# Performance work log

Hardware: AMD Instinct MI355X
Metric: run time of the kernel (lower is better)

Reference implementation:

```python
import jax, jax.numpy as jnp
import numpy as np

N, D, IN_DIM, H, L = 20000, 32, 3, 64, 3


def _lstm_agg(h_nodes, nbr_sorted, W_ih, W_hh, b_ih, b_hh):
    """Batched LSTM over each node's (sorted) neighbor sequence; returns final hidden state h_T."""
    n = h_nodes.shape[0]
    hidden = W_hh.shape[1]

    def step(carry, idx):
        h, c = carry
        x = h_nodes[idx]                                     # [N, in_d] irregular gather
        gates = x @ W_ih.T + h @ W_hh.T + b_ih + b_hh        # [N, 4H], torch gate order i,f,g,o
        i_g, f_g, g_g, o_g = jnp.split(gates, 4, axis=-1)
        c = jax.nn.sigmoid(f_g) * c + jax.nn.sigmoid(i_g) * jnp.tanh(g_g)
        h = jax.nn.sigmoid(o_g) * jnp.tanh(c)
        return (h, c), None

    init = (jnp.zeros((n, hidden), h_nodes.dtype), jnp.zeros((n, hidden), h_nodes.dtype))
    (h_T, _), _ = jax.lax.scan(step, init, nbr_sorted.T)      # scan over D neighbor slots
    return h_T


def _layer(h, nbr_sorted, W_ih, W_hh, b_ih, b_hh, Wl, bl):
    agg = _lstm_agg(h, nbr_sorted, W_ih, W_hh, b_ih, b_hh)    # [N, H]
    comb = jnp.concatenate([h, agg], axis=-1)                 # [N, in_d + H]
    return jax.nn.relu(comb @ Wl.T + bl)


def _forward(node_features, nbr, params, W_out, b_out):
    nbr_sorted = jnp.sort(nbr, axis=1)   # permutation-invariant ordering (Eq. 9)
    h = node_features
    for p in params:
        h = _layer(h, nbr_sorted, *p)
    return (h @ W_out.T + b_out).squeeze(-1)   # [N] per-node log-likelihood scores


def setup_inputs():
    key = jax.random.key(0)
    ks = jax.random.split(key, 40)
    inp = {}
    inp["node_features"] = jax.random.normal(ks[0], (N, IN_DIM), jnp.float32)
    inp["nbr"] = jax.random.randint(ks[1], (N, D), 0, N, jnp.int32)
    k = 2
    s = 1.0 / np.sqrt(H)
    for l in range(L):
        in_d = IN_DIM if l == 0 else H
        inp[f"W_ih{l}"] = (jax.random.normal(ks[k], (4 * H, in_d)) * (1.0 / np.sqrt(in_d))).astype(jnp.float32); k += 1
        inp[f"W_hh{l}"] = (jax.random.normal(ks[k], (4 * H, H)) * s).astype(jnp.float32); k += 1
        inp[f"b_ih{l}"] = (jax.random.normal(ks[k], (4 * H,)) * s).astype(jnp.float32); k += 1
        inp[f"b_hh{l}"] = (jax.random.normal(ks[k], (4 * H,)) * s).astype(jnp.float32); k += 1
        inp[f"Wl{l}"] = (jax.random.normal(ks[k], (H, in_d + H)) * (1.0 / np.sqrt(in_d + H))).astype(jnp.float32); k += 1
        inp[f"bl{l}"] = (jax.random.normal(ks[k], (H,)) * s).astype(jnp.float32); k += 1
    inp["W_out"] = (jax.random.normal(ks[k], (1, H)) * s).astype(jnp.float32); k += 1
    inp["b_out"] = jnp.zeros((1,), jnp.float32)
    return inp


def reference(node_features, nbr, W_ih0, W_hh0, b_ih0, b_hh0, Wl0, bl0, W_ih1, W_hh1, b_ih1, b_hh1, Wl1, bl1, W_ih2, W_hh2, b_ih2, b_hh2, Wl2, bl2, W_out, b_out):
    params = [
        (W_ih0, W_hh0, b_ih0, b_hh0, Wl0, bl0),
        (W_ih1, W_hh1, b_ih1, b_hh1, Wl1, bl1),
        (W_ih2, W_hh2, b_ih2, b_hh2, Wl2, bl2),
    ]
    return _forward(node_features, nbr, params, W_out, b_out)
```

## Files before the change

kernel.cpp:

```cpp
#include <hip/hip_runtime.h>
#include <hip/hip_bf16.h>

#define NN 20000
#define NG 1250
#define LOG2E 1.44269504088896f
#define TWOLOG2E 2.88539008177793f

typedef __attribute__((ext_vector_type(8))) short short8;
typedef __attribute__((ext_vector_type(4))) float floatx4;

__device__ __forceinline__ floatx4 MF(short8 a, short8 b, floatx4 c) {
    return __builtin_amdgcn_mfma_f32_16x16x32_bf16(a, b, c, 0, 0, 0);
}
__device__ __forceinline__ float ex2(float x) { return __builtin_amdgcn_exp2f(x); }
__device__ __forceinline__ float rcp(float x) { return __builtin_amdgcn_rcpf(x); }
__device__ __forceinline__ float clamp30(float x) {
    return __builtin_fminf(__builtin_fmaxf(x, -30.f), 30.f);
}
__device__ __forceinline__ unsigned short bf16r(float x) {
    return __builtin_bit_cast(unsigned short, __float2bfloat16(x));
}
__device__ __forceinline__ void lds_barrier() {
    asm volatile("s_waitcnt lgkmcnt(0)\n\ts_barrier" ::: "memory");
}
__device__ __forceinline__ int rowswz(int L) {
    return L ^ (((L >> 4) & 1) << 1) ^ ((L >> 3) & 1);
}

__device__ __forceinline__ void lstm_cell4(const floatx4* acc, float* cst,
                                           unsigned short* buf, int q, int u) {
    #pragma unroll
    for (int r = 0; r < 4; r++) {
        float gi = clamp30(acc[0][r]);
        float gf = clamp30(acc[1][r]);
        float gg = clamp30(acc[2][r]);
        float go = clamp30(acc[3][r]);
        float ei = ex2(-gi), ef = ex2(-gf), eg = ex2(-gg), eo = ex2(-go);
        float pf = 1.f + ef;
        float p  = (1.f + ei) * (1.f + eg);
        float num = fmaf(cst[r], p, (1.f - eg) * pf);
        float cm  = num * rcp(p * pf);
        cst[r] = cm;
        float ec = ex2(-clamp30(TWOLOG2E * cm));
        float h  = (1.f - ec) * rcp((1.f + eo) * (1.f + ec));
        int row = 4*q + r + 16*(u >> 3);
        buf[rowswz(row)*8 + (u & 7)] = bf16r(h);
    }
}

#define PREP_TOT (49152 + 49152 + 12288 + 12288 + 768 + 640000)
__global__ void prep_kernel(const float* __restrict__ x, const int* __restrict__ nbr,
    const float* __restrict__ Wih0, const float* __restrict__ Whh0,
    const float* __restrict__ bih0, const float* __restrict__ bhh0, const float* __restrict__ Wl0,
    const float* __restrict__ Wih1, const float* __restrict__ Whh1,
    const float* __restrict__ bih1, const float* __restrict__ bhh1, const float* __restrict__ Wl1,
    const float* __restrict__ Wih2, const float* __restrict__ Whh2,
    const float* __restrict__ bih2, const float* __restrict__ bhh2, const float* __restrict__ Wl2,
    unsigned short* __restrict__ Wih_p, unsigned short* __restrict__ Whh_p,
    unsigned short* __restrict__ Wlx_p, unsigned short* __restrict__ Wlh_p,
    float* __restrict__ bsum, unsigned short* __restrict__ x32, int* __restrict__ nbrT)
{
    int tid = blockIdx.x * 256 + threadIdx.x;
    if (tid < NN) {
        int v[32];
        const int4* src = (const int4*)(nbr + tid * 32);
        #pragma unroll
        for (int i = 0; i < 8; i++) {
            int4 t = src[i];
            v[4*i] = t.x; v[4*i+1] = t.y; v[4*i+2] = t.z; v[4*i+3] = t.w;
        }
        #pragma unroll
        for (int k = 2; k <= 32; k <<= 1)
            #pragma unroll
            for (int j = k >> 1; j > 0; j >>= 1)
                #pragma unroll
                for (int i = 0; i < 32; i++) {
                    int ixj = i ^ j;
                    if (ixj > i) {
                        bool up = (i & k) == 0;
                        int a = v[i], b = v[ixj];
                        bool sw = up ? (a > b) : (a < b);
                        if (sw) { v[i] = b; v[ixj] = a; }
                    }
                }
        int g = tid >> 4, m = tid & 15;
        int base = g * 512 + m;
        #pragma unroll
        for (int t = 0; t < 32; t++) nbrT[base + t * 16] = v[t];
    }
    for (int i = blockIdx.x * 256 + threadIdx.x; i < PREP_TOT; i += gridDim.x * 256) {
        int j = i;
        if (j < 49152) {
            int l = j >> 14, e = j & 16383;
            if (l == 0) {
                if (e < 8192) {
                    int col = e >> 5, k = e & 31;
                    float sc = (col >= 128 && col < 192) ? TWOLOG2E : LOG2E;
                    float v = (k < 3) ? Wih0[col*3 + k] * sc : 0.f;
                    Wih_p[e] = bf16r(v);
                }
            } else {
                int col = e >> 6, k = e & 63;
                const float* W = (l == 1) ? Wih1 : Wih2;
                float sc = (col >= 128 && col < 192) ? TWOLOG2E : LOG2E;
                Wih_p[l*16384 + e] = bf16r(W[col*64 + k] * sc);
            }
            continue;
        }
        j -= 49152;
        if (j < 49152) {
            int l = j >> 14, e = j & 16383;
            int col = e >> 6, k = e & 63;
            const float* W = (l == 0) ? Whh0 : ((l == 1) ? Whh1 : Whh2);
            float sc = (col >= 128 && col < 192) ? TWOLOG2E : LOG2E;
            Whh_p[l*16384 + e] = bf16r(W[col*64 + k] * sc);
            continue;
        }
        j -= 49152;
        if (j < 12288) {
            int l = j >> 12, e = j & 4095;
            if (l == 0) {
                if (e < 2048) {
                    int col = e >> 5, k = e & 31;
                    float v = (k < 3) ? Wl0[col*67 + k] : 0.f;
                    Wlx_p[e] = bf16r(v);
                }
            } else {
                int col = e >> 6, k = e & 63;
                const float* W = (l == 1) ? Wl1 : Wl2;
                Wlx_p[l*4096 + e] = bf16r(W[col*128 + k]);
            }
            continue;
        }
        j -= 12288;
        if (j < 12288) {
            int l = j >> 12, e = j & 4095;
            int col = e >> 6, k = e & 63;
            float v = (l == 0) ? Wl0[col*67 + 3 + k]
                               : ((l == 1) ? Wl1 : Wl2)[col*128 + 64 + k];
            Wlh_p[l*4096 + e] = bf16r(v);
            continue;
        }
        j -= 12288;
        if (j < 768) {
            int l = j >> 8, col = j & 255;
            const float* bi = (l == 0) ? bih0 : ((l == 1) ? bih1 : bih2);
            const float* bh = (l == 0) ? bhh0 : ((l == 1) ? bhh1 : bhh2);
            float sc = (col >= 128 && col < 192) ? TWOLOG2E : LOG2E;
            bsum[l*256 + col] = (bi[col] + bh[col]) * sc;
            continue;
        }
        j -= 768;
        {
            int n = j >> 5, k = j & 31;
            x32[j] = bf16r((k < 3) ? x[n*3 + k] : 0.f);
        }
    }
}

template<int XKC, int LASTL>
__global__ __launch_bounds__(256, 3)
void lstm_mfma_kernel(const unsigned short* __restrict__ xsrc,
                      const int* __restrict__ nbrT,
                      const unsigned short* __restrict__ Wih,
                      const unsigned short* __restrict__ Whh,
                      const float* __restrict__ bsum,
                      const unsigned short* __restrict__ Wlx,
                      const unsigned short* __restrict__ Wlh,
                      const float* __restrict__ bl,
                      const float* __restrict__ W_out,
                      const float* __restrict__ b_out,
                      void* __restrict__ hout)
{
    __shared__ unsigned short sA[2][1024];
    __shared__ float sRed[64];

    const int w    = threadIdx.x >> 6;
    const int lane = threadIdx.x & 63;
    const int q    = lane >> 4;
    const int c    = lane & 15;
    const int XS   = XKC * 32;

    const int g = blockIdx.x;
    const int node0 = g * 16;
    const int* nbg = nbrT + g * 512;

    short8 fWih[4][XKC];
    short8 fWhh[4][2];
    float  biasv[4];
    #pragma unroll
    for (int t4 = 0; t4 < 4; t4++) {
        int col = 64*t4 + 16*w + c;
        biasv[t4] = bsum[col];
        #pragma unroll
        for (int kc = 0; kc < XKC; kc++)
            fWih[t4][kc] = *(const short8*)(Wih + col*XS + kc*32 + q*8);
        fWhh[t4][0] = *(const short8*)(Whh + col*64 + q*8);
        fWhh[t4][1] = *(const short8*)(Whh + col*64 + 32 + q*8);
    }

    int idx = nbg[c];
    short8 xg[XKC];
    #pragma unroll
    for (int kc = 0; kc < XKC; kc++)
        xg[kc] = *(const short8*)(xsrc + (long)idx * XS + kc*32 + q*8);

    floatx4 acc[4];
    #pragma unroll
    for (int t4 = 0; t4 < 4; t4++) {
        floatx4 bb; bb[0] = biasv[t4]; bb[1] = biasv[t4]; bb[2] = biasv[t4]; bb[3] = biasv[t4];
        acc[t4] = MF(xg[0], fWih[t4][0], bb);
        if (XKC == 2) acc[t4] = MF(xg[1], fWih[t4][1], acc[t4]);
    }
    idx = nbg[16 + c];
    #pragma unroll
    for (int kc = 0; kc < XKC; kc++)
        xg[kc] = *(const short8*)(xsrc + (long)idx * XS + kc*32 + q*8);
    int idx2 = nbg[32 + c];

    float cst[4] = {0.f, 0.f, 0.f, 0.f};
    short8 hA[2];
    const int u = 16*w + c;

    #pragma unroll 1
    for (int t = 0; t < 32; t++) {
        if (t > 0) {
            #pragma unroll
            for (int t4 = 0; t4 < 4; t4++) {
                acc[t4] = MF(hA[0], fWhh[t4][0], acc[t4]);
                acc[t4] = MF(hA[1], fWhh[t4][1], acc[t4]);
            }
        }
        unsigned short* buf = sA[(t + 1) & 1];
        lstm_cell4(acc, cst, buf, q, u);

        if (t < 31) {
            #pragma unroll
            for (int t4 = 0; t4 < 4; t4++) {
                floatx4 bb; bb[0] = biasv[t4]; bb[1] = biasv[t4]; bb[2] = biasv[t4]; bb[3] = biasv[t4];
                acc[t4] = MF(xg[0], fWih[t4][0], bb);
                if (XKC == 2) acc[t4] = MF(xg[1], fWih[t4][1], acc[t4]);
            }
            if (t < 30) {
                #pragma unroll
                for (int kc = 0; kc < XKC; kc++)
                    xg[kc] = *(const short8*)(xsrc + (long)idx2 * XS + kc*32 + q*8);
                int tn = (t + 3 < 32) ? t + 3 : 31;
                idx2 = nbg[tn*16 + c];
            }
        }
        lds_barrier();
        const unsigned short* rd = sA[(t + 1) & 1];
        hA[0] = *(const short8*)(rd + rowswz(lane)*8);
        hA[1] = *(const short8*)(rd + 512 + rowswz(lane)*8);
    }

    const int col = 16*w + c;
    short8 fx[XKC], fh0, fh1;
    float blv = bl[col];
    #pragma unroll
    for (int kc = 0; kc < XKC; kc++)
        fx[kc] = *(const short8*)(Wlx + col*XS + kc*32 + q*8);
    fh0 = *(const short8*)(Wlh + col*64 + q*8);
    fh1 = *(const short8*)(Wlh + col*64 + 32 + q*8);
    short8 hin[XKC];
    #pragma unroll
    for (int kc = 0; kc < XKC; kc++)
        hin[kc] = *(const short8*)(xsrc + (long)(node0 + c) * XS + kc*32 + q*8);

    floatx4 a; a[0] = blv; a[1] = blv; a[2] = blv; a[3] = blv;
    #pragma unroll
    for (int kc = 0; kc < XKC; kc++) a = MF(hin[kc], fx[kc], a);
    a = MF(hA[0], fh0, a);
    a = MF(hA[1], fh1, a);

    if (!LASTL) {
        #pragma unroll
        for (int r = 0; r < 4; r++)
            ((unsigned short*)hout)[(node0 + 4*q + r) * 64 + col] = bf16r(fmaxf(a[r], 0.f));
    } else {
        float wo = W_out[col];
        float p[4];
        #pragma unroll
        for (int r = 0; r < 4; r++) p[r] = fmaxf(a[r], 0.f) * wo;
        #pragma unroll
        for (int d = 1; d < 16; d <<= 1) {
            #pragma unroll
            for (int r = 0; r < 4; r++) p[r] += __shfl_xor(p[r], d);
        }
        if (c == 0) {
            #pragma unroll
            for (int r = 0; r < 4; r++) sRed[w*16 + 4*q + r] = p[r];
        }
        lds_barrier();
        if (w == 0 && lane < 16)
            ((float*)hout)[node0 + lane] =
                sRed[lane] + sRed[16 + lane] + sRed[32 + lane] + sRed[48 + lane] + b_out[0];
    }
}

extern "C" void kernel_launch(void* const* d_in, const int* in_sizes, int n_in,
                              void* d_out, int out_size, void* d_ws, size_t ws_size,
                              hipStream_t stream) {
    (void)in_sizes; (void)n_in; (void)out_size; (void)ws_size;
    const float* node_features = (const float*)d_in[0];
    const int*   nbr           = (const int*)d_in[1];
    const float* Wih[3] = {(const float*)d_in[2],  (const float*)d_in[8],  (const float*)d_in[14]};
    const float* Whh[3] = {(const float*)d_in[3],  (const float*)d_in[9],  (const float*)d_in[15]};
    const float* bih[3] = {(const float*)d_in[4],  (const float*)d_in[10], (const float*)d_in[16]};
    const float* bhh[3] = {(const float*)d_in[5],  (const float*)d_in[11], (const float*)d_in[17]};
    const float* Wl[3]  = {(const float*)d_in[6],  (const float*)d_in[12], (const float*)d_in[18]};
    const float* bl[3]  = {(const float*)d_in[7],  (const float*)d_in[13], (const float*)d_in[19]};
    const float* W_out  = (const float*)d_in[20];
    const float* b_out  = (const float*)d_in[21];

    char* ws = (char*)d_ws;
    int*            nbrT  = (int*)ws;
    unsigned short* x32   = (unsigned short*)(ws + 2560000);
    unsigned short* hb1   = (unsigned short*)(ws + 3840000);
    unsigned short* hb2   = (unsigned short*)(ws + 6400000);
    unsigned short* Wih_p = (unsigned short*)(ws + 8960000);
    unsigned short* Whh_p = (unsigned short*)(ws + 9058304);
    unsigned short* Wlx_p = (unsigned short*)(ws + 9156608);
    unsigned short* Wlh_p = (unsigned short*)(ws + 9181184);
    float*          bsum  = (float*)(ws + 9205760);

    prep_kernel<<<1024, 256, 0, stream>>>(node_features, nbr,
        Wih[0], Whh[0], bih[0], bhh[0], Wl[0],
        Wih[1], Whh[1], bih[1], bhh[1], Wl[1],
        Wih[2], Whh[2], bih[2], bhh[2], Wl[2],
        Wih_p, Whh_p, Wlx_p, Wlh_p, bsum, x32, nbrT);

    lstm_mfma_kernel<1, 0><<<NG, 256, 0, stream>>>(x32, nbrT,
        Wih_p,         Whh_p,         bsum,       Wlx_p,        Wlh_p,        bl[0],
        nullptr, nullptr, hb1);
    lstm_mfma_kernel<2, 0><<<NG, 256, 0, stream>>>(hb1, nbrT,
        Wih_p + 16384, Whh_p + 16384, bsum + 256, Wlx_p + 4096, Wlh_p + 4096, bl[1],
        nullptr, nullptr, hb2);
    lstm_mfma_kernel<2, 1><<<NG, 256, 0, stream>>>(hb2, nbrT,
        Wih_p + 32768, Whh_p + 32768, bsum + 512, Wlx_p + 8192, Wlh_p + 8192, bl[2],
        W_out, b_out, (float*)d_out);
}
```

Measured before the change: 323.9 us.

## Halve LSTM block to two waves, each computing 32 hidden units per gate

Result: slower. 349.9 us (+8.0%).

```diff
diff --git a/kernel.cpp b/kernel.cpp
--- a/kernel.cpp
+++ b/kernel.cpp
@@ -27,28 +27,7 @@
     return L ^ (((L >> 4) & 1) << 1) ^ ((L >> 3) & 1);
 }
 
-__device__ __forceinline__ void lstm_cell4(const floatx4* acc, float* cst,
-                                           unsigned short* buf, int q, int u) {
-    #pragma unroll
-    for (int r = 0; r < 4; r++) {
-        float gi = clamp30(acc[0][r]);
-        float gf = clamp30(acc[1][r]);
-        float gg = clamp30(acc[2][r]);
-        float go = clamp30(acc[3][r]);
-        float ei = ex2(-gi), ef = ex2(-gf), eg = ex2(-gg), eo = ex2(-go);
-        float pf = 1.f + ef;
-        float p  = (1.f + ei) * (1.f + eg);
-        float num = fmaf(cst[r], p, (1.f - eg) * pf);
-        float cm  = num * rcp(p * pf);
-        cst[r] = cm;
-        float ec = ex2(-clamp30(TWOLOG2E * cm));
-        float h  = (1.f - ec) * rcp((1.f + eo) * (1.f + ec));
-        int row = 4*q + r + 16*(u >> 3);
-        buf[rowswz(row)*8 + (u & 7)] = bf16r(h);
-    }
-}
-
-#define PREP_TOT (49152 + 49152 + 12288 + 12288 + 768 + 640000)
+#define PREP_TOT (40960 + 49152 + 12288 + 12288 + 768 + 640000)
 __global__ void prep_kernel(const float* __restrict__ x, const int* __restrict__ nbr,
     const float* __restrict__ Wih0, const float* __restrict__ Whh0,
     const float* __restrict__ bih0, const float* __restrict__ bhh0, const float* __restrict__ Wl0,
@@ -90,24 +69,26 @@
     }
     for (int i = blockIdx.x * 256 + threadIdx.x; i < PREP_TOT; i += gridDim.x * 256) {
         int j = i;
-        if (j < 49152) {
-            int l = j >> 14, e = j & 16383;
-            if (l == 0) {
-                if (e < 8192) {
-                    int col = e >> 5, k = e & 31;
-                    float sc = (col >= 128 && col < 192) ? TWOLOG2E : LOG2E;
-                    float v = (k < 3) ? Wih0[col*3 + k] * sc : 0.f;
-                    Wih_p[e] = bf16r(v);
-                }
+        if (j < 40960) {
+            if (j < 8192) {
+                int jL = j & 7, lane = (j >> 3) & 63, t = (j >> 9) & 7, w = (j >> 12) & 1;
+                int col = 64*(t>>1) + 32*w + 16*(t&1) + (lane & 15);
+                int k   = (lane >> 4)*8 + jL;
+                float sc = ((t>>1) == 2) ? TWOLOG2E : LOG2E;
+                Wih_p[j] = bf16r((k < 3) ? Wih0[col*3 + k] * sc : 0.f);
             } else {
-                int col = e >> 6, k = e & 63;
+                int jj = j - 8192; int l = (jj >> 14) + 1; jj &= 16383;
+                int jL = jj & 7, lane = (jj >> 3) & 63, kc = (jj >> 9) & 1;
+                int t = (jj >> 10) & 7, w = (jj >> 13) & 1;
+                int col = 64*(t>>1) + 32*w + 16*(t&1) + (lane & 15);
+                int k   = kc*32 + (lane >> 4)*8 + jL;
                 const float* W = (l == 1) ? Wih1 : Wih2;
-                float sc = (col >= 128 && col < 192) ? TWOLOG2E : LOG2E;
-                Wih_p[l*16384 + e] = bf16r(W[col*64 + k] * sc);
-            }
-            continue;
-        }
-        j -= 49152;
+                float sc = ((t>>1) == 2) ? TWOLOG2E : LOG2E;
+                Wih_p[j] = bf16r(W[col*64 + k] * sc);
+            }
+            continue;
+        }
+        j -= 40960;
         if (j < 49152) {
             int l = j >> 14, e = j & 16383;
             int col = e >> 6, k = e & 63;
@@ -159,7 +140,7 @@
 }
 
 template<int XKC, int LASTL>
-__global__ __launch_bounds__(256, 3)
+__global__ __launch_bounds__(128, 2)
 void lstm_mfma_kernel(const unsigned short* __restrict__ xsrc,
                       const int* __restrict__ nbrT,
                       const unsigned short* __restrict__ Wih,
@@ -173,7 +154,7 @@
                       void* __restrict__ hout)
 {
     __shared__ unsigned short sA[2][1024];
-    __shared__ float sRed[64];
+    __shared__ float sRed[4][16];
 
     const int w    = threadIdx.x >> 6;
     const int lane = threadIdx.x & 63;
@@ -185,19 +166,20 @@
     const int node0 = g * 16;
     const int* nbg = nbrT + g * 512;
 
-    short8 fWih[4][XKC];
-    short8 fWhh[4][2];
-    float  biasv[4];
-    #pragma unroll
-    for (int t4 = 0; t4 < 4; t4++) {
-        int col = 64*t4 + 16*w + c;
-        biasv[t4] = bsum[col];
+    short8 fWih[8][XKC];
+    short8 fWhh[8][2];
+    float  biasv[8];
+    #pragma unroll
+    for (int t = 0; t < 8; t++) {
+        int col = 64*(t>>1) + 32*w + 16*(t&1) + c;
+        biasv[t] = bsum[col];
         #pragma unroll
         for (int kc = 0; kc < XKC; kc++)
-            fWih[t4][kc] = *(const short8*)(Wih + col*XS + kc*32 + q*8);
-        fWhh[t4][0] = *(const short8*)(Whh + col*64 + q*8);
-        fWhh[t4][1] = *(const short8*)(Whh + col*64 + 32 + q*8);
-    }
+            fWih[t][kc] = *(const short8*)(Wih + ((w*8 + t)*XKC + kc)*512 + lane*8);
+        fWhh[t][0] = *(const short8*)(Whh + col*64 + q*8);
+        fWhh[t][1] = *(const short8*)(Whh + col*64 + 32 + q*8);
+    }
+    floatx4 zeroC = {0.f, 0.f, 0.f, 0.f};
 
     int idx = nbg[c];
     short8 xg[XKC];
@@ -205,12 +187,11 @@
     for (int kc = 0; kc < XKC; kc++)
         xg[kc] = *(const short8*)(xsrc + (long)idx * XS + kc*32 + q*8);
 
-    floatx4 acc[4];
-    #pragma unroll
-    for (int t4 = 0; t4 < 4; t4++) {
-        floatx4 bb; bb[0] = biasv[t4]; bb[1] = biasv[t4]; bb[2] = biasv[t4]; bb[3] = biasv[t4];
-        acc[t4] = MF(xg[0], fWih[t4][0], bb);
-        if (XKC == 2) acc[t4] = MF(xg[1], fWih[t4][1], acc[t4]);
+    floatx4 acc[8];
+    #pragma unroll
+    for (int t = 0; t < 8; t++) {
+        acc[t] = MF(xg[0], fWih[t][0], zeroC);
+        if (XKC == 2) acc[t] = MF(xg[1], fWih[t][1], acc[t]);
     }
     idx = nbg[16 + c];
     #pragma unroll
@@ -218,28 +199,45 @@
         xg[kc] = *(const short8*)(xsrc + (long)idx * XS + kc*32 + q*8);
     int idx2 = nbg[32 + c];
 
-    float cst[4] = {0.f, 0.f, 0.f, 0.f};
+    float cst[8] = {0.f,0.f,0.f,0.f,0.f,0.f,0.f,0.f};
     short8 hA[2];
-    const int u = 16*w + c;
 
     #pragma unroll 1
     for (int t = 0; t < 32; t++) {
         if (t > 0) {
             #pragma unroll
-            for (int t4 = 0; t4 < 4; t4++) {
-                acc[t4] = MF(hA[0], fWhh[t4][0], acc[t4]);
-                acc[t4] = MF(hA[1], fWhh[t4][1], acc[t4]);
+            for (int t8 = 0; t8 < 8; t8++) {
+                acc[t8] = MF(hA[0], fWhh[t8][0], acc[t8]);
+                acc[t8] = MF(hA[1], fWhh[t8][1], acc[t8]);
             }
         }
         unsigned short* buf = sA[(t + 1) & 1];
-        lstm_cell4(acc, cst, buf, q, u);
-
+        #pragma unroll
+        for (int s = 0; s < 2; s++) {
+            const int u = 32*w + 16*s + c;
+            #pragma unroll
+            for (int r = 0; r < 4; r++) {
+                float gi = clamp30(acc[0 + s][r] + biasv[0 + s]);
+                float gf = clamp30(acc[2 + s][r] + biasv[2 + s]);
+                float gg = clamp30(acc[4 + s][r] + biasv[4 + s]);
+                float go = clamp30(acc[6 + s][r] + biasv[6 + s]);
+                float ei = ex2(-gi), ef = ex2(-gf), eg = ex2(-gg), eo = ex2(-go);
+                float pf = 1.f + ef;
+                float p  = (1.f + ei) * (1.f + eg);
+                float num = fmaf(cst[4*s + r], p, (1.f - eg) * pf);
+                float cm  = num * rcp(p * pf);
+                cst[4*s + r] = cm;
+                float ec = ex2(-clamp30(TWOLOG2E * cm));
+                float h  = (1.f - ec) * rcp((1.f + eo) * (1.f + ec));
+                int row = 4*q + r + 16*(u >> 3);
+                buf[rowswz(row)*8 + (u & 7)] = bf16r(h);
+            }
+        }
         if (t < 31) {
             #pragma unroll
-            for (int t4 = 0; t4 < 4; t4++) {
-                floatx4 bb; bb[0] = biasv[t4]; bb[1] = biasv[t4]; bb[2] = biasv[t4]; bb[3] = biasv[t4];
-                acc[t4] = MF(xg[0], fWih[t4][0], bb);
-                if (XKC == 2) acc[t4] = MF(xg[1], fWih[t4][1], acc[t4]);
+            for (int t8 = 0; t8 < 8; t8++) {
+                acc[t8] = MF(xg[0], fWih[t8][0], zeroC);
+                if (XKC == 2) acc[t8] = MF(xg[1], fWih[t8][1], acc[t8]);
             }
             if (t < 30) {
                 #pragma unroll
@@ -255,47 +253,52 @@
         hA[1] = *(const short8*)(rd + 512 + rowswz(lane)*8);
     }
 
-    const int col = 16*w + c;
-    short8 fx[XKC], fh0, fh1;
-    float blv = bl[col];
-    #pragma unroll
-    for (int kc = 0; kc < XKC; kc++)
-        fx[kc] = *(const short8*)(Wlx + col*XS + kc*32 + q*8);
-    fh0 = *(const short8*)(Wlh + col*64 + q*8);
-    fh1 = *(const short8*)(Wlh + col*64 + 32 + q*8);
     short8 hin[XKC];
     #pragma unroll
     for (int kc = 0; kc < XKC; kc++)
         hin[kc] = *(const short8*)(xsrc + (long)(node0 + c) * XS + kc*32 + q*8);
 
-    floatx4 a; a[0] = blv; a[1] = blv; a[2] = blv; a[3] = blv;
-    #pragma unroll
-    for (int kc = 0; kc < XKC; kc++) a = MF(hin[kc], fx[kc], a);
-    a = MF(hA[0], fh0, a);
-    a = MF(hA[1], fh1, a);
-
-    if (!LASTL) {
-        #pragma unroll
-        for (int r = 0; r < 4; r++)
-            ((unsigned short*)hout)[(node0 + 4*q + r) * 64 + col] = bf16r(fmaxf(a[r], 0.f));
-    } else {
-        float wo = W_out[col];
-        float p[4];
-        #pragma unroll
-        for (int r = 0; r < 4; r++) p[r] = fmaxf(a[r], 0.f) * wo;
-        #pragma unroll
-        for (int d = 1; d < 16; d <<= 1) {
-            #pragma unroll
-            for (int r = 0; r < 4; r++) p[r] += __shfl_xor(p[r], d);
-        }
-        if (c == 0) {
-            #pragma unroll
-            for (int r = 0; r < 4; r++) sRed[w*16 + 4*q + r] = p[r];
-        }
+    #pragma unroll
+    for (int s = 0; s < 2; s++) {
+        int col = 32*w + 16*s + c;
+        float blv = bl[col];
+        floatx4 a; a[0] = blv; a[1] = blv; a[2] = blv; a[3] = blv;
+        short8 fx0 = *(const short8*)(Wlx + col*XS + q*8);
+        a = MF(hin[0], fx0, a);
+        if (XKC == 2) {
+            short8 fx1 = *(const short8*)(Wlx + col*XS + 32 + q*8);
+            a = MF(hin[1], fx1, a);
+        }
+        short8 fh0 = *(const short8*)(Wlh + col*64 + q*8);
+        short8 fh1 = *(const short8*)(Wlh + col*64 + 32 + q*8);
+        a = MF(hA[0], fh0, a);
+        a = MF(hA[1], fh1, a);
+
+        if (!LASTL) {
+            #pragma unroll
+            for (int r = 0; r < 4; r++)
+                ((unsigned short*)hout)[(node0 + 4*q + r) * 64 + col] = bf16r(fmaxf(a[r], 0.f));
+        } else {
+            float wo = W_out[col];
+            float pr[4];
+            #pragma unroll
+            for (int r = 0; r < 4; r++) pr[r] = fmaxf(a[r], 0.f) * wo;
+            #pragma unroll
+            for (int d = 1; d < 16; d <<= 1) {
+                #pragma unroll
+                for (int r = 0; r < 4; r++) pr[r] += __shfl_xor(pr[r], d);
+            }
+            if (c == 0) {
+                #pragma unroll
+                for (int r = 0; r < 4; r++) sRed[2*w + s][4*q + r] = pr[r];
+            }
+        }
+    }
+    if (LASTL) {
         lds_barrier();
         if (w == 0 && lane < 16)
             ((float*)hout)[node0 + lane] =
-                sRed[lane] + sRed[16 + lane] + sRed[32 + lane] + sRed[48 + lane] + b_out[0];
+                sRed[0][lane] + sRed[1][lane] + sRed[2][lane] + sRed[3][lane] + b_out[0];
     }
 }
 
@@ -320,10 +323,10 @@
     unsigned short* hb1   = (unsigned short*)(ws + 3840000);
     unsigned short* hb2   = (unsigned short*)(ws + 6400000);
     unsigned short* Wih_p = (unsigned short*)(ws + 8960000);
-    unsigned short* Whh_p = (unsigned short*)(ws + 9058304);
-    unsigned short* Wlx_p = (unsigned short*)(ws + 9156608);
-    unsigned short* Wlh_p = (unsigned short*)(ws + 9181184);
-    float*          bsum  = (float*)(ws + 9205760);
+    unsigned short* Whh_p = (unsigned short*)(ws + 9041920);
+    unsigned short* Wlx_p = (unsigned short*)(ws + 9140224);
+    unsigned short* Wlh_p = (unsigned short*)(ws + 9164800);
+    float*          bsum  = (float*)(ws + 9189376);
 
     prep_kernel<<<1024, 256, 0, stream>>>(node_features, nbr,
         Wih[0], Whh[0], bih[0], bhh[0], Wl[0],
@@ -331,13 +334,13 @@
         Wih[2], Whh[2], bih[2], bhh[2], Wl[2],
         Wih_p, Whh_p, Wlx_p, Wlh_p, bsum, x32, nbrT);
 
-    lstm_mfma_kernel<1, 0><<<NG, 256, 0, stream>>>(x32, nbrT,
-        Wih_p,         Whh_p,         bsum,       Wlx_p,        Wlh_p,        bl[0],
+    lstm_mfma_kernel<1, 0><<<NG, 128, 0, stream>>>(x32, nbrT,
+        Wih_p,          Whh_p,         bsum,       Wlx_p,        Wlh_p,        bl[0],
         nullptr, nullptr, hb1);
-    lstm_mfma_kernel<2, 0><<<NG, 256, 0, stream>>>(hb1, nbrT,
-        Wih_p + 16384, Whh_p + 16384, bsum + 256, Wlx_p + 4096, Wlh_p + 4096, bl[1],
+    lstm_mfma_kernel<2, 0><<<NG, 128, 0, stream>>>(hb1, nbrT,
+        Wih_p + 8192,   Whh_p + 16384, bsum + 256, Wlx_p + 4096, Wlh_p + 4096, bl[1],
         nullptr, nullptr, hb2);
-    lstm_mfma_kernel<2, 1><<<NG, 256, 0, stream>>>(hb2, nbrT,
-        Wih_p + 32768, Whh_p + 32768, bsum + 512, Wlx_p + 8192, Wlh_p + 8192, bl[2],
+    lstm_mfma_kernel<2, 1><<<NG, 128, 0, stream>>>(hb2, nbrT,
+        Wih_p + 24576,  Whh_p + 32768, bsum + 512, Wlx_p + 8192, Wlh_p + 8192, bl[2],
         W_out, b_out, (float*)d_out);
 }
```
